# Kernel tuning notes

Measured on AMD Instinct MI355X. Metric: run time of the kernel, lower is better.

## Reference

```python
import jax, jax.numpy as jnp
import numpy as np

L = 2048
E = 1024
H = 16
D = E // H


def setup_inputs() -> dict:
    key = jax.random.key(0)
    ks = jax.random.split(key, 9)
    inp = {
        "values": jax.random.normal(ks[0], (L, E), dtype=jnp.float32),
        "keys": jax.random.normal(ks[1], (L, E), dtype=jnp.float32),
        "query": jax.random.normal(ks[2], (L, E), dtype=jnp.float32),
        "dist_matrix": jax.random.uniform(ks[3], (L, L), dtype=jnp.float32),
        "Wv": jax.random.normal(ks[4], (E, E), dtype=jnp.float32) * 0.02,
        "Wk": jax.random.normal(ks[5], (E, E), dtype=jnp.float32) * 0.02,
        "Wq": jax.random.normal(ks[6], (E, E), dtype=jnp.float32) * 0.02,
        "Wo": jax.random.normal(ks[7], (E, E), dtype=jnp.float32) * 0.02,
        "bo": jax.random.normal(ks[8], (E,), dtype=jnp.float32) * 0.02,
    }
    return inp


def reference(values, keys, query, dist_matrix, Wv, Wk, Wq, Wo, bo):
    # Linear projections (torch Linear: x @ W.T), then split heads: [L, H, D]
    v = (values @ Wv.T).reshape(L, H, D)
    k = (keys @ Wk.T).reshape(L, H, D)
    q = (query @ Wq.T).reshape(L, H, D)

    # energy: [H, Lq, Lk]
    energy = jnp.einsum("qhd,khd->hqk", q, k)

    # distance bias: zeros -> inf, then 1/(d+1); broadcast over heads
    dm = jnp.where(dist_matrix == 0, jnp.inf, dist_matrix)
    bias = 1.0 / (dm + 1.0)
    energy = energy + bias[None, :, :]

    attn = jax.nn.softmax(energy / jnp.sqrt(jnp.float32(E)), axis=2)

    out = jnp.einsum("hql,lhd->qhd", attn, v).reshape(L, H * D)
    return out @ Wo.T + bo
```

## Files before the change

### kernel.cpp

```cpp
#include <hip/hip_runtime.h>


#define L_SEQ 2048
#define E_DIM 1024
#define H_HEADS 16
#define D_HEAD 64
#define KSPLIT 4
#define OSPLIT 2

typedef unsigned short u16;
typedef unsigned int u32;
typedef __attribute__((ext_vector_type(8))) short bf16x8;
typedef __attribute__((ext_vector_type(4))) short bf16x4;
typedef __attribute__((ext_vector_type(8))) unsigned short u16x8;
typedef __attribute__((ext_vector_type(4))) unsigned short u16x4;
typedef __attribute__((ext_vector_type(4))) float f32x4;

#define C_LOG2E_32 0.045084220027780106f

#if __has_builtin(__builtin_amdgcn_mfma_f32_16x16x16bf16_1k)
#define HAVE_MFMA16 1
#else
#define HAVE_MFMA16 0
#endif

__device__ __forceinline__ float bf2f(u16 u) {
  union { u32 i; float f; } v; v.i = ((u32)u) << 16; return v.f;
}
__device__ __forceinline__ u16 f2bf(float f) {
  union { float f; u32 i; } v; v.f = f;
  u32 u = v.i;
  u += 0x7FFFu + ((u >> 16) & 1u);
  return (u16)(u >> 16);
}
__device__ __forceinline__ u32 pack_bf16_pair(float lo, float hi) {
  union { float f; u32 u; } a, b;
  a.f = lo; b.f = hi;
  return __builtin_amdgcn_perm(b.u + 0x8000u, a.u + 0x8000u, 0x07060302u);
}
__device__ __forceinline__ void gload16(const u16* g, u16* l) {
  __builtin_amdgcn_global_load_lds(
      (const __attribute__((address_space(1))) u32*)g,
      (__attribute__((address_space(3))) u32*)l, 16, 0, 0);
}

__global__ void cvt_all(const float* __restrict__ xq, const float* __restrict__ xk,
                        const float* __restrict__ xv,
                        const float* __restrict__ wq, const float* __restrict__ wk,
                        const float* __restrict__ wv, const float* __restrict__ wo,
                        const float* __restrict__ dist, const float* __restrict__ bo,
                        u16* oq, u16* ok, u16* ov,
                        u16* owq, u16* owk, u16* owv, u16* owo, u16* obias,
                        float* __restrict__ outp)
{
  size_t gid = (size_t)blockIdx.x * 256 + threadIdx.x;
  const size_t NQ = 524288;
  const size_t NW = 262144;
  const size_t DL = 1048576;
  const size_t FILL = 3 * NQ + 4 * NW + DL;

  if (gid >= FILL) {
    size_t off = (gid - FILL) * 4;
    int n = (int)(off & (E_DIM - 1));
    *(f32x4*)&outp[off] = *(const f32x4*)&bo[n];
    return;
  }

  const float* src; u16* dst; size_t off; bool isb = false;
  if      (gid <     NQ)           { src = xq;   dst = oq;    off = gid; }
  else if (gid < 2 * NQ)           { src = xk;   dst = ok;    off = gid - NQ; }
  else if (gid < 3 * NQ)           { src = xv;   dst = ov;    off = gid - 2 * NQ; }
  else if (gid < 3 * NQ + NW)      { src = wq;   dst = owq;   off = gid - 3 * NQ; }
  else if (gid < 3 * NQ + 2 * NW)  { src = wk;   dst = owk;   off = gid - 3 * NQ - NW; }
  else if (gid < 3 * NQ + 3 * NW)  { src = wv;   dst = owv;   off = gid - 3 * NQ - 2 * NW; }
  else if (gid < 3 * NQ + 4 * NW)  { src = wo;   dst = owo;   off = gid - 3 * NQ - 3 * NW; }
  else { src = dist; dst = obias; off = gid - 3 * NQ - 4 * NW; isb = true; }

  f32x4 v = *(const f32x4*)&src[off * 4];
  u16x4 o;
#pragma unroll
  for (int j = 0; j < 4; ++j) {
    float f = v[j];
    if (isb) f = (f == 0.f) ? 0.f : C_LOG2E_32 / (f + 1.f);
    o[j] = f2bf(f);
  }
  *(u16x4*)&dst[off * 4] = o;
}

#define TM 128
#define TN 128
#define BK 32

template<int OUTMODE>
__global__ __launch_bounds__(256, 3) void gemm_pd(
    const u16* __restrict__ A0, const u16* __restrict__ B0, void* __restrict__ C0,
    const u16* __restrict__ A1, const u16* __restrict__ B1, void* __restrict__ C1,
    const u16* __restrict__ A2, const u16* __restrict__ B2, void* __restrict__ C2,
    int M, int N, int K)
{
  const u16* A; const u16* B; void* C;
  if (OUTMODE == 2)         { A = A0; B = B0; C = C0; }
  else if (blockIdx.z == 0) { A = A0; B = B0; C = C0; }
  else if (blockIdx.z == 1) { A = A1; B = B1; C = C1; }
  else                      { A = A2; B = B2; C = C2; }

  __shared__ __align__(16) u16 As[2][TM * BK];
  __shared__ __align__(16) u16 Bs[2][TN * BK];

  const int m0 = blockIdx.y * TM;
  const int n0 = blockIdx.x * TN;
  const int t = threadIdx.x;
  const int wave = t >> 6;
  const int lane = t & 63;
  const int quad = lane >> 4;
  const int col  = lane & 15;
  const int wm = (wave >> 1) * 64;
  const int wn = (wave & 1) * 64;

  const int roff = lane >> 2;
  const int gcol = ((lane & 3) ^ ((lane >> 3) & 3)) * 8;
  const u16* gA = A + (size_t)(m0 + wave * 32 + roff) * K + gcol;
  const u16* gB = B + (size_t)(n0 + wave * 32 + roff) * K + gcol;
  const int lo0 = (wave * 32) * BK;
  const int lo1 = (wave * 32 + 16) * BK;

  const int kbeg = (OUTMODE == 2) ? blockIdx.z * (K / OSPLIT) : 0;
  const int kend = (OUTMODE == 2) ? kbeg + K / OSPLIT : K;

  f32x4 acc[4][4];
#pragma unroll
  for (int i = 0; i < 4; ++i)
#pragma unroll
    for (int j = 0; j < 4; ++j) acc[i][j] = (f32x4){0.f, 0.f, 0.f, 0.f};

  gload16(gA + kbeg, &As[0][lo0]);
  gload16(gA + (size_t)16 * K + kbeg, &As[0][lo1]);
  gload16(gB + kbeg, &Bs[0][lo0]);
  gload16(gB + (size_t)16 * K + kbeg, &Bs[0][lo1]);

  const int slot8 = (quad ^ ((col >> 1) & 3)) * 8;

  int buf = 0;
  for (int k0 = kbeg; k0 < kend; k0 += BK) {
    __syncthreads();
    int nk = k0 + BK;
    if (nk < kend) {
      gload16(gA + nk, &As[buf ^ 1][lo0]);
      gload16(gA + (size_t)16 * K + nk, &As[buf ^ 1][lo1]);
      gload16(gB + nk, &Bs[buf ^ 1][lo0]);
      gload16(gB + (size_t)16 * K + nk, &Bs[buf ^ 1][lo1]);
    }

    bf16x8 af[4], bfr[4];
#pragma unroll
    for (int i = 0; i < 4; ++i)
      af[i] = *(const bf16x8*)&As[buf][(wm + i * 16 + col) * BK + slot8];
#pragma unroll
    for (int j = 0; j < 4; ++j)
      bfr[j] = *(const bf16x8*)&Bs[buf][(wn + j * 16 + col) * BK + slot8];

#pragma unroll
    for (int i = 0; i < 4; ++i)
#pragma unroll
      for (int j = 0; j < 4; ++j)
        acc[i][j] = __builtin_amdgcn_mfma_f32_16x16x32_bf16(af[i], bfr[j], acc[i][j], 0, 0, 0);

    buf ^= 1;
  }

  const bool transC = (OUTMODE == 0) && (blockIdx.z == 2);
#pragma unroll
  for (int i = 0; i < 4; ++i) {
    int rowb = m0 + wm + i * 16 + quad * 4;
#pragma unroll
    for (int j = 0; j < 4; ++j) {
      int cn = n0 + wn + j * 16 + col;
      if (OUTMODE == 2) {
#pragma unroll
        for (int r = 0; r < 4; ++r)
          unsafeAtomicAdd(&((float*)C)[(size_t)(rowb + r) * N + cn], acc[i][j][r]);
      } else if (transC) {
        u16x4 pk;
#pragma unroll
        for (int r = 0; r < 4; ++r) pk[r] = f2bf(acc[i][j][r]);
        *(u16x4*)&((u16*)C)[(size_t)cn * M + rowb] = pk;
      } else {
#pragma unroll
        for (int r = 0; r < 4; ++r)
          ((u16*)C)[(size_t)(rowb + r) * N + cn] = f2bf(acc[i][j][r]);
      }
    }
  }
}

#define FK 64
#define LDV 72

__global__ __launch_bounds__(256, 6) void flash4(
    const u16* __restrict__ Q, const u16* __restrict__ Kp,
    const u16* __restrict__ Vt, const u16* __restrict__ Bb,
    u16* __restrict__ Op, float* __restrict__ lp)
{
  __shared__ __align__(16) u16 Ks[FK][LDV];
  __shared__ __align__(16) u16 Vs[D_HEAD][LDV];
#if !HAVE_MFMA16
  __shared__ __align__(16) u16 Ps[4][16][LDV];
#endif

  const int h  = blockIdx.y;
  const int q0 = blockIdx.x * 64;
  const int z  = blockIdx.z;
  const int hoff = h * D_HEAD;
  const int kbase = z * (L_SEQ / KSPLIT);
  const int t = threadIdx.x;
  const int wave = t >> 6;
  const int lane = t & 63;
  const int quad = lane >> 4;
  const int col  = lane & 15;

  bf16x8 qf[2];
  {
    const u16* qrow = Q + (size_t)(q0 + wave * 16 + col) * E_DIM + hoff;
    qf[0] = *(const bf16x8*)(qrow + quad * 8);
    qf[1] = *(const bf16x8*)(qrow + 32 + quad * 8);
  }

  float l_lane = 0.f;
  f32x4 oacc[4];
#pragma unroll
  for (int td = 0; td < 4; ++td) oacc[td] = (f32x4){0.f, 0.f, 0.f, 0.f};

  const u16* brow = Bb + (size_t)(q0 + wave * 16 + col) * L_SEQ;
  const int cst = t & 7, rst = t >> 3;

  for (int kt = 0; kt < L_SEQ / KSPLIT / FK; ++kt) {
    const int k0 = kbase + kt * FK;
    __syncthreads();
#pragma unroll
    for (int s = 0; s < 2; ++s) {
      int rr = rst + s * 32;
      *(u16x8*)&Ks[rr][cst * 8] = *(const u16x8*)&Kp[(size_t)(k0 + rr) * E_DIM + hoff + cst * 8];
      *(u16x8*)&Vs[rr][cst * 8] = *(const u16x8*)&Vt[(size_t)(hoff + rr) * L_SEQ + k0 + cst * 8];
    }
    float pb[4][4];
#pragma unroll
    for (int tt = 0; tt < 4; ++tt) {
      u16x4 bv = *(const u16x4*)&brow[k0 + tt * 16 + quad * 4];
#pragma unroll
      for (int r = 0; r < 4; ++r) pb[tt][r] = bf2f(bv[r]);
    }
    __syncthreads();

#pragma unroll
    for (int tt = 0; tt < 4; ++tt) {
      f32x4 a = (f32x4){0.f, 0.f, 0.f, 0.f};
      a = __builtin_amdgcn_mfma_f32_16x16x32_bf16(*(const bf16x8*)&Ks[tt * 16 + col][quad * 8], qf[0], a, 0, 0, 0);
      a = __builtin_amdgcn_mfma_f32_16x16x32_bf16(*(const bf16x8*)&Ks[tt * 16 + col][32 + quad * 8], qf[1], a, 0, 0, 0);
      float p[4];
#pragma unroll
      for (int r = 0; r < 4; ++r) {
        p[r] = __builtin_amdgcn_exp2f(fmaf(a[r], C_LOG2E_32, pb[tt][r]));
        l_lane += p[r];
      }
#if HAVE_MFMA16
      union { u32 u[2]; bf16x4 v; } pk;
      pk.u[0] = pack_bf16_pair(p[0], p[1]);
      pk.u[1] = pack_bf16_pair(p[2], p[3]);
#pragma unroll
      for (int td = 0; td < 4; ++td) {
        bf16x4 vf = *(const bf16x4*)&Vs[td * 16 + col][tt * 16 + quad * 4];
        oacc[td] = __builtin_amdgcn_mfma_f32_16x16x16bf16_1k(vf, pk.v, oacc[td], 0, 0, 0);
      }
#else
      uint2 w;
      w.x = pack_bf16_pair(p[0], p[1]);
      w.y = pack_bf16_pair(p[2], p[3]);
      *(uint2*)&Ps[wave][col][tt * 16 + quad * 4] = w;
#endif
    }

#if !HAVE_MFMA16
#pragma unroll
    for (int kk = 0; kk < 2; ++kk) {
      bf16x8 pf = *(const bf16x8*)&Ps[wave][col][kk * 32 + quad * 8];
#pragma unroll
      for (int td = 0; td < 4; ++td) {
        bf16x8 vf = *(const bf16x8*)&Vs[td * 16 + col][kk * 32 + quad * 8];
        oacc[td] = __builtin_amdgcn_mfma_f32_16x16x32_bf16(pf, vf, oacc[td], 0, 0, 0);
      }
    }
#endif
  }

  l_lane += __shfl_xor(l_lane, 16);
  l_lane += __shfl_xor(l_lane, 32);
  if (lane < 16)
    lp[((size_t)z * L_SEQ + q0 + wave * 16 + lane) * H_HEADS + h] = l_lane;

#if HAVE_MFMA16
  const int qmine = q0 + wave * 16 + col;
#pragma unroll
  for (int td = 0; td < 4; ++td) {
    u16x4 pk;
#pragma unroll
    for (int r = 0; r < 4; ++r) pk[r] = f2bf(oacc[td][r]);
    *(u16x4*)&Op[((size_t)z * L_SEQ + qmine) * E_DIM + hoff + td * 16 + quad * 4] = pk;
  }
#else
  const int qrow_mine = q0 + wave * 16 + quad * 4;
#pragma unroll
  for (int td = 0; td < 4; ++td)
#pragma unroll
    for (int r = 0; r < 4; ++r)
      Op[((size_t)z * L_SEQ + qrow_mine + r) * E_DIM + hoff + td * 16 + col] = f2bf(oacc[td][r]);
#endif
}

__global__ void merge_attn(const u16* __restrict__ Op, const float* __restrict__ lp,
                           u16* __restrict__ AOb)
{
  size_t gid = (size_t)blockIdx.x * 256 + threadIdx.x;
  size_t idx = gid * 4;
  int q = (int)(idx >> 10);
  int e = (int)(idx & 1023);
  int h = e >> 6;
  float o[4] = {0.f, 0.f, 0.f, 0.f};
  float lsum = 0.f;
#pragma unroll
  for (int s = 0; s < KSPLIT; ++s) {
    u16x4 pv = *(const u16x4*)&Op[((size_t)s * L_SEQ + q) * E_DIM + e];
#pragma unroll
    for (int j = 0; j < 4; ++j) o[j] += bf2f(pv[j]);
    lsum += lp[((size_t)s * L_SEQ + q) * H_HEADS + h];
  }
  float inv = 1.f / lsum;
  u16x4 pk;
#pragma unroll
  for (int j = 0; j < 4; ++j) pk[j] = f2bf(o[j] * inv);
  *(u16x4*)&AOb[idx] = pk;
}

extern "C" void kernel_launch(void* const* d_in, const int* in_sizes, int n_in,
                              void* d_out, int out_size, void* d_ws, size_t ws_size,
                              hipStream_t stream)
{
  const float* values = (const float*)d_in[0];
  const float* keys   = (const float*)d_in[1];
  const float* query  = (const float*)d_in[2];
  const float* dist   = (const float*)d_in[3];
  const float* Wv     = (const float*)d_in[4];
  const float* Wk     = (const float*)d_in[5];
  const float* Wq     = (const float*)d_in[6];
  const float* Wo     = (const float*)d_in[7];
  const float* bo     = (const float*)d_in[8];
  float* out = (float*)d_out;

  const size_t MB = (size_t)1 << 20;
  char* w = (char*)d_ws;
  u16* xq  = (u16*)(w + 0 * MB);
  u16* xk  = (u16*)(w + 4 * MB);
  u16* xv  = (u16*)(w + 8 * MB);
  u16* wqb = (u16*)(w + 12 * MB);
  u16* wkb = (u16*)(w + 14 * MB);
  u16* wvb = (u16*)(w + 16 * MB);
  u16* wob = (u16*)(w + 18 * MB);
  u16* Bb  = (u16*)(w + 20 * MB);
  u16* Qh  = (u16*)(w + 28 * MB);
  u16* Kh  = (u16*)(w + 32 * MB);
  u16* Vth = (u16*)(w + 36 * MB);
  u16* AOb = (u16*)(w + 40 * MB);
  float* lp = (float*)(w + 44 * MB);
  u16* Op  = (u16*)(w + 0 * MB);

  cvt_all<<<16384, 256, 0, stream>>>(query, keys, values, Wq, Wk, Wv, Wo, dist, bo,
                                     xq, xk, xv, wqb, wkb, wvb, wob, Bb, out);

  dim3 gProj(E_DIM / TN, L_SEQ / TM, 3);
  gemm_pd<0><<<gProj, 256, 0, stream>>>(xq, wqb, Qh,
                                        xk, wkb, Kh,
                                        xv, wvb, Vth,
                                        L_SEQ, E_DIM, E_DIM);

  dim3 gAttn(L_SEQ / 64, H_HEADS, KSPLIT);
  flash4<<<gAttn, 256, 0, stream>>>(Qh, Kh, Vth, Bb, Op, lp);

  merge_attn<<<(L_SEQ * E_DIM / 4) / 256, 256, 0, stream>>>(Op, lp, AOb);

  dim3 gOut(E_DIM / TN, L_SEQ / TM, OSPLIT);
  gemm_pd<2><<<gOut, 256, 0, stream>>>(AOb, wob, out,
                                       AOb, wob, out,
                                       AOb, wob, out,
                                       L_SEQ, E_DIM, E_DIM);
}
```

Baseline: 221.8 us.

## Double-buffer attention K/V via async LDS loads and shrink GEMM M-tile

The attention kernel now streams K and V tiles with global_load_lds into double-buffered, XOR-swizzled shared memory and prefetches the bias for the next tile. This removes one barrier per iteration and overlaps loads with MFMA work. The K tile drops to 32 keys and P is always staged through LDS for the 16x16x32 MFMA path, removing the 16x16x16 path. The projection GEMM tile shrinks from 128x128 to 64x128 with a higher occupancy hint, giving more blocks at the cost of less reuse per block.

```diff
diff --git a/kernel.cpp b/kernel.cpp
--- a/kernel.cpp
+++ b/kernel.cpp
@@ -11,18 +11,11 @@
 typedef unsigned short u16;
 typedef unsigned int u32;
 typedef __attribute__((ext_vector_type(8))) short bf16x8;
-typedef __attribute__((ext_vector_type(4))) short bf16x4;
 typedef __attribute__((ext_vector_type(8))) unsigned short u16x8;
 typedef __attribute__((ext_vector_type(4))) unsigned short u16x4;
 typedef __attribute__((ext_vector_type(4))) float f32x4;
 
 #define C_LOG2E_32 0.045084220027780106f
-
-#if __has_builtin(__builtin_amdgcn_mfma_f32_16x16x16bf16_1k)
-#define HAVE_MFMA16 1
-#else
-#define HAVE_MFMA16 0
-#endif
 
 __device__ __forceinline__ float bf2f(u16 u) {
   union { u32 i; float f; } v; v.i = ((u32)u) << 16; return v.f;
@@ -87,12 +80,12 @@
   *(u16x4*)&dst[off * 4] = o;
 }
 
-#define TM 128
+#define TM 64
 #define TN 128
 #define BK 32
 
 template<int OUTMODE>
-__global__ __launch_bounds__(256, 3) void gemm_pd(
+__global__ __launch_bounds__(256, 4) void gemm_pd(
     const u16* __restrict__ A0, const u16* __restrict__ B0, void* __restrict__ C0,
     const u16* __restrict__ A1, const u16* __restrict__ B1, void* __restrict__ C1,
     const u16* __restrict__ A2, const u16* __restrict__ B2, void* __restrict__ C2,
@@ -114,29 +107,30 @@
   const int lane = t & 63;
   const int quad = lane >> 4;
   const int col  = lane & 15;
-  const int wm = (wave >> 1) * 64;
+  const int wm = (wave >> 1) * 32;
   const int wn = (wave & 1) * 64;
 
-  const int roff = lane >> 2;
-  const int gcol = ((lane & 3) ^ ((lane >> 3) & 3)) * 8;
-  const u16* gA = A + (size_t)(m0 + wave * 32 + roff) * K + gcol;
-  const u16* gB = B + (size_t)(n0 + wave * 32 + roff) * K + gcol;
-  const int lo0 = (wave * 32) * BK;
-  const int lo1 = (wave * 32 + 16) * BK;
+  const int sr = lane >> 2;
+  const int sg = ((lane & 3) ^ ((lane >> 3) & 3)) * 8;
+  const u16* gA  = A + (size_t)(m0 + wave * 16 + sr) * K + sg;
+  const u16* gB0 = B + (size_t)(n0 + wave * 16 + sr) * K + sg;
+  const u16* gB1 = B + (size_t)(n0 + 64 + wave * 16 + sr) * K + sg;
+  const int lA  = (wave * 16) * BK;
+  const int lB0 = (wave * 16) * BK;
+  const int lB1 = (64 + wave * 16) * BK;
 
   const int kbeg = (OUTMODE == 2) ? blockIdx.z * (K / OSPLIT) : 0;
   const int kend = (OUTMODE == 2) ? kbeg + K / OSPLIT : K;
 
-  f32x4 acc[4][4];
-#pragma unroll
-  for (int i = 0; i < 4; ++i)
+  f32x4 acc[2][4];
+#pragma unroll
+  for (int i = 0; i < 2; ++i)
 #pragma unroll
     for (int j = 0; j < 4; ++j) acc[i][j] = (f32x4){0.f, 0.f, 0.f, 0.f};
 
-  gload16(gA + kbeg, &As[0][lo0]);
-  gload16(gA + (size_t)16 * K + kbeg, &As[0][lo1]);
-  gload16(gB + kbeg, &Bs[0][lo0]);
-  gload16(gB + (size_t)16 * K + kbeg, &Bs[0][lo1]);
+  gload16(gA + kbeg, &As[0][lA]);
+  gload16(gB0 + kbeg, &Bs[0][lB0]);
+  gload16(gB1 + kbeg, &Bs[0][lB1]);
 
   const int slot8 = (quad ^ ((col >> 1) & 3)) * 8;
 
@@ -145,22 +139,21 @@
     __syncthreads();
     int nk = k0 + BK;
     if (nk < kend) {
-      gload16(gA + nk, &As[buf ^ 1][lo0]);
-      gload16(gA + (size_t)16 * K + nk, &As[buf ^ 1][lo1]);
-      gload16(gB + nk, &Bs[buf ^ 1][lo0]);
-      gload16(gB + (size_t)16 * K + nk, &Bs[buf ^ 1][lo1]);
-    }
-
-    bf16x8 af[4], bfr[4];
-#pragma unroll
-    for (int i = 0; i < 4; ++i)
+      gload16(gA + nk, &As[buf ^ 1][lA]);
+      gload16(gB0 + nk, &Bs[buf ^ 1][lB0]);
+      gload16(gB1 + nk, &Bs[buf ^ 1][lB1]);
+    }
+
+    bf16x8 af[2], bfr[4];
+#pragma unroll
+    for (int i = 0; i < 2; ++i)
       af[i] = *(const bf16x8*)&As[buf][(wm + i * 16 + col) * BK + slot8];
 #pragma unroll
     for (int j = 0; j < 4; ++j)
       bfr[j] = *(const bf16x8*)&Bs[buf][(wn + j * 16 + col) * BK + slot8];
 
 #pragma unroll
-    for (int i = 0; i < 4; ++i)
+    for (int i = 0; i < 2; ++i)
 #pragma unroll
       for (int j = 0; j < 4; ++j)
         acc[i][j] = __builtin_amdgcn_mfma_f32_16x16x32_bf16(af[i], bfr[j], acc[i][j], 0, 0, 0);
@@ -170,7 +163,7 @@
 
   const bool transC = (OUTMODE == 0) && (blockIdx.z == 2);
 #pragma unroll
-  for (int i = 0; i < 4; ++i) {
+  for (int i = 0; i < 2; ++i) {
     int rowb = m0 + wm + i * 16 + quad * 4;
 #pragma unroll
     for (int j = 0; j < 4; ++j) {
@@ -193,25 +186,24 @@
   }
 }
 
-#define FK 64
-#define LDV 72
-
-__global__ __launch_bounds__(256, 6) void flash4(
+#define FK 32
+#define PLDV 40
+
+__global__ __launch_bounds__(256, 7) void flash5(
     const u16* __restrict__ Q, const u16* __restrict__ Kp,
     const u16* __restrict__ Vt, const u16* __restrict__ Bb,
     u16* __restrict__ Op, float* __restrict__ lp)
 {
-  __shared__ __align__(16) u16 Ks[FK][LDV];
-  __shared__ __align__(16) u16 Vs[D_HEAD][LDV];
-#if !HAVE_MFMA16
-  __shared__ __align__(16) u16 Ps[4][16][LDV];
-#endif
+  __shared__ __align__(16) u16 Ks[2][FK * 64];
+  __shared__ __align__(16) u16 Vs[2][D_HEAD * FK];
+  __shared__ __align__(16) u16 Ps[4][16][PLDV];
 
   const int h  = blockIdx.y;
   const int q0 = blockIdx.x * 64;
   const int z  = blockIdx.z;
   const int hoff = h * D_HEAD;
   const int kbase = z * (L_SEQ / KSPLIT);
+  const int NT = (L_SEQ / KSPLIT) / FK;
   const int t = threadIdx.x;
   const int wave = t >> 6;
   const int lane = t & 63;
@@ -225,71 +217,76 @@
     qf[1] = *(const bf16x8*)(qrow + 32 + quad * 8);
   }
 
+  const int krow = wave * 8 + (lane >> 3);
+  const int kg = ((lane & 7) ^ (lane >> 3)) * 8;
+  const u16* gK = Kp + (size_t)krow * E_DIM + hoff + kg;
+  u16* lK = &Ks[0][wave * 8 * 64];
+
+  const int vrow = wave * 16 + (lane >> 2);
+  const int vg = ((lane & 3) ^ ((lane >> 4) & 3)) * 8;
+  const u16* gV = Vt + (size_t)(hoff + vrow) * L_SEQ + vg;
+  u16* lV = &Vs[0][wave * 16 * FK];
+
   float l_lane = 0.f;
   f32x4 oacc[4];
 #pragma unroll
   for (int td = 0; td < 4; ++td) oacc[td] = (f32x4){0.f, 0.f, 0.f, 0.f};
 
   const u16* brow = Bb + (size_t)(q0 + wave * 16 + col) * L_SEQ;
-  const int cst = t & 7, rst = t >> 3;
-
-  for (int kt = 0; kt < L_SEQ / KSPLIT / FK; ++kt) {
+
+  gload16(gK + (size_t)kbase * E_DIM, lK);
+  gload16(gV + kbase, lV);
+  u16x4 bv[2], bn[2] = {(u16x4){0,0,0,0}, (u16x4){0,0,0,0}};
+  bv[0] = *(const u16x4*)&brow[kbase + quad * 4];
+  bv[1] = *(const u16x4*)&brow[kbase + 16 + quad * 4];
+
+  const int ks0 = (quad ^ (col & 7)) * 8;
+  const int ks1 = ((quad + 4) ^ (col & 7)) * 8;
+  const int vsl = (quad ^ ((col >> 2) & 3)) * 8;
+
+  int buf = 0;
+  for (int kt = 0; kt < NT; ++kt) {
     const int k0 = kbase + kt * FK;
     __syncthreads();
-#pragma unroll
-    for (int s = 0; s < 2; ++s) {
-      int rr = rst + s * 32;
-      *(u16x8*)&Ks[rr][cst * 8] = *(const u16x8*)&Kp[(size_t)(k0 + rr) * E_DIM + hoff + cst * 8];
-      *(u16x8*)&Vs[rr][cst * 8] = *(const u16x8*)&Vt[(size_t)(hoff + rr) * L_SEQ + k0 + cst * 8];
-    }
-    float pb[4][4];
-#pragma unroll
-    for (int tt = 0; tt < 4; ++tt) {
-      u16x4 bv = *(const u16x4*)&brow[k0 + tt * 16 + quad * 4];
-#pragma unroll
-      for (int r = 0; r < 4; ++r) pb[tt][r] = bf2f(bv[r]);
-    }
-    __syncthreads();
-
-#pragma unroll
-    for (int tt = 0; tt < 4; ++tt) {
+    if (kt + 1 < NT) {
+      const int nk = k0 + FK;
+      gload16(gK + (size_t)nk * E_DIM, lK + (buf ^ 1 ? 0 : 0) + (buf ^ 1) * (FK * 64) - buf * 0);
+      gload16(gV + nk, lV + (buf ^ 1) * (D_HEAD * FK));
+      bn[0] = *(const u16x4*)&brow[nk + quad * 4];
+      bn[1] = *(const u16x4*)&brow[nk + 16 + quad * 4];
+    }
+    const u16* Kb = &Ks[buf][0];
+    const u16* Vb = &Vs[buf][0];
+
+#pragma unroll
+    for (int tt = 0; tt < 2; ++tt) {
+      const u16* kr = &Kb[(tt * 16 + col) * 64];
       f32x4 a = (f32x4){0.f, 0.f, 0.f, 0.f};
-      a = __builtin_amdgcn_mfma_f32_16x16x32_bf16(*(const bf16x8*)&Ks[tt * 16 + col][quad * 8], qf[0], a, 0, 0, 0);
-      a = __builtin_amdgcn_mfma_f32_16x16x32_bf16(*(const bf16x8*)&Ks[tt * 16 + col][32 + quad * 8], qf[1], a, 0, 0, 0);
+      a = __builtin_amdgcn_mfma_f32_16x16x32_bf16(*(const bf16x8*)&kr[ks0], qf[0], a, 0, 0, 0);
+      a = __builtin_amdgcn_mfma_f32_16x16x32_bf16(*(const bf16x8*)&kr[ks1], qf[1], a, 0, 0, 0);
       float p[4];
 #pragma unroll
       for (int r = 0; r < 4; ++r) {
-        p[r] = __builtin_amdgcn_exp2f(fmaf(a[r], C_LOG2E_32, pb[tt][r]));
+        p[r] = __builtin_amdgcn_exp2f(fmaf(a[r], C_LOG2E_32, bf2f(bv[tt][r])));
         l_lane += p[r];
       }
-#if HAVE_MFMA16
-      union { u32 u[2]; bf16x4 v; } pk;
-      pk.u[0] = pack_bf16_pair(p[0], p[1]);
-      pk.u[1] = pack_bf16_pair(p[2], p[3]);
-#pragma unroll
-      for (int td = 0; td < 4; ++td) {
-        bf16x4 vf = *(const bf16x4*)&Vs[td * 16 + col][tt * 16 + quad * 4];
-        oacc[td] = __builtin_amdgcn_mfma_f32_16x16x16bf16_1k(vf, pk.v, oacc[td], 0, 0, 0);
-      }
-#else
       uint2 w;
       w.x = pack_bf16_pair(p[0], p[1]);
       w.y = pack_bf16_pair(p[2], p[3]);
       *(uint2*)&Ps[wave][col][tt * 16 + quad * 4] = w;
-#endif
-    }
-
-#if !HAVE_MFMA16
-#pragma unroll
-    for (int kk = 0; kk < 2; ++kk) {
-      bf16x8 pf = *(const bf16x8*)&Ps[wave][col][kk * 32 + quad * 8];
+    }
+
+    {
+      bf16x8 pf = *(const bf16x8*)&Ps[wave][col][quad * 8];
 #pragma unroll
       for (int td = 0; td < 4; ++td) {
-        bf16x8 vf = *(const bf16x8*)&Vs[td * 16 + col][kk * 32 + quad * 8];
+        bf16x8 vf = *(const bf16x8*)&Vb[(td * 16 + col) * FK + vsl];
         oacc[td] = __builtin_amdgcn_mfma_f32_16x16x32_bf16(pf, vf, oacc[td], 0, 0, 0);
       }
     }
-#endif
+
+    bv[0] = bn[0]; bv[1] = bn[1];
+    buf ^= 1;
   }
 
   l_lane += __shfl_xor(l_lane, 16);
@@ -297,23 +294,12 @@
   if (lane < 16)
     lp[((size_t)z * L_SEQ + q0 + wave * 16 + lane) * H_HEADS + h] = l_lane;
 
-#if HAVE_MFMA16
-  const int qmine = q0 + wave * 16 + col;
-#pragma unroll
-  for (int td = 0; td < 4; ++td) {
-    u16x4 pk;
-#pragma unroll
-    for (int r = 0; r < 4; ++r) pk[r] = f2bf(oacc[td][r]);
-    *(u16x4*)&Op[((size_t)z * L_SEQ + qmine) * E_DIM + hoff + td * 16 + quad * 4] = pk;
-  }
-#else
   const int qrow_mine = q0 + wave * 16 + quad * 4;
 #pragma unroll
   for (int td = 0; td < 4; ++td)
 #pragma unroll
     for (int r = 0; r < 4; ++r)
       Op[((size_t)z * L_SEQ + qrow_mine + r) * E_DIM + hoff + td * 16 + col] = f2bf(oacc[td][r]);
-#endif
 }
 
 __global__ void merge_attn(const u16* __restrict__ Op, const float* __restrict__ lp,
@@ -382,7 +368,7 @@
                                         L_SEQ, E_DIM, E_DIM);
 
   dim3 gAttn(L_SEQ / 64, H_HEADS, KSPLIT);
-  flash4<<<gAttn, 256, 0, stream>>>(Qh, Kh, Vth, Bb, Op, lp);
+  flash5<<<gAttn, 256, 0, stream>>>(Qh, Kh, Vth, Bb, Op, lp);
 
   merge_attn<<<(L_SEQ * E_DIM / 4) / 256, 256, 0, stream>>>(Op, lp, AOb);
 
```

Result: faster. 217.4 us (-2.0%).
